# Kernel tuning notes

Hardware: AMD Instinct MI355X
Metric: run time of the kernel (lower is better)

## Reference

```python
import jax, jax.numpy as jnp
import numpy as np

N = 50000      # nodes
E = 1_600_000  # edges
F_IN = 128; HID = 128; LAT = 64; OUT = 128; GEN = 2


def gcn_conv(x, src, dst, norm, W, b, n_nodes):
    """PyG GCNConv with self-loops already appended to (src, dst) and
    symmetric normalization `norm` precomputed per edge."""
    h = x @ W                                    # [N, out]
    msg = h[src] * norm[:, None]                 # [E+N, out] gather + scale
    out = jax.ops.segment_sum(msg, dst, num_segments=n_nodes)
    return out + b


def _self_loop_norm(edge_index, n_nodes):
    loops = jnp.arange(n_nodes, dtype=edge_index.dtype)
    src = jnp.concatenate([edge_index[0], loops])
    dst = jnp.concatenate([edge_index[1], loops])
    deg = jnp.zeros((n_nodes,), jnp.float32).at[dst].add(1.0)
    dinv = jnp.where(deg > 0, deg ** -0.5, 0.0)
    norm = dinv[src] * dinv[dst]
    return src, dst, norm


def setup_inputs() -> dict:
    key = jax.random.key(0)
    ks = jax.random.split(key, 12)
    p = lambda k, s: jax.random.normal(k, s, jnp.float32) * 0.05
    return {
        "x": jax.random.normal(ks[0], (N, F_IN), jnp.float32),
        "edge_index": jax.random.randint(ks[1], (2, E), 0, N, jnp.int32),
        "eps": jax.random.normal(ks[2], (N, LAT), jnp.float32),
        "u": jax.random.uniform(ks[3], (N, GEN), jnp.float32),
        "W1": p(ks[4], (F_IN, HID)), "b1": jnp.zeros((HID,), jnp.float32),
        "W_mu": p(ks[5], (HID, LAT)), "b_mu": jnp.zeros((LAT,), jnp.float32),
        "W_ls": p(ks[6], (HID, LAT)), "b_ls": jnp.zeros((LAT,), jnp.float32),
        "W_dx": p(ks[7], (LAT, OUT)), "b_dx": jnp.zeros((OUT,), jnp.float32),
        "W_g": p(ks[8], (LAT, GEN)), "b_g": jnp.zeros((GEN,), jnp.float32),
        "W_lc": p(ks[9], (LAT, 1)), "b_lc": jnp.zeros((1,), jnp.float32),
    }


def reference(x, edge_index, eps, u, W1, b1, W_mu, b_mu, W_ls, b_ls,
              W_dx, b_dx, W_g, b_g, W_lc, b_lc):
    n = x.shape[0]
    src, dst, norm = _self_loop_norm(edge_index, n)

    # Encoder: GCN -> relu -> (mu, logvar)
    h = jax.nn.relu(gcn_conv(x, src, dst, norm, W1, b1, n))
    mu = gcn_conv(h, src, dst, norm, W_mu, b_mu, n)
    logvar = gcn_conv(h, src, dst, norm, W_ls, b_ls, n)

    # reparameterize: z = eps * exp(0.5*logvar) + mu
    z = eps * jnp.exp(0.5 * logvar) + mu

    # decoders / classifiers
    recon_x = gcn_conv(z, src, dst, norm, W_dx, b_dx, n)
    logits_gender = gcn_conv(z, src, dst, norm, W_g, b_g, n)
    logits_label = z @ W_lc + b_lc

    # Gumbel-softmax (hard, straight-through), temperature=1.0
    g = -jnp.log(-jnp.log(u + 1e-20) + 1e-20)
    y_soft = jax.nn.softmax(logits_gender + g, axis=-1)
    y_hard = jax.nn.one_hot(jnp.argmax(y_soft, axis=-1), GEN, dtype=y_soft.dtype)
    gender = jax.lax.stop_gradient(y_hard - y_soft) + y_soft

    return (recon_x, gender, logits_label, mu, logvar, z)
```

## Files before the change

### kernel.cpp

```cpp
#include <hip/hip_runtime.h>
#include <hip/hip_fp16.h>
#include <cstddef>


constexpr int R = 200;
constexpr int NBUCK = 250;
constexpr int NBLK = 250;
constexpr int SLABCAP = 12288;

__global__ __launch_bounds__(256) void hist_kernel(
    const int* __restrict__ dst, int* __restrict__ gh, int e, int chunk) {
  __shared__ int h[NBUCK];
  for (int t = threadIdx.x; t < NBUCK; t += 256) h[t] = 0;
  __syncthreads();
  int beg = blockIdx.x * chunk;
  int fin = min(e, beg + chunk);
  for (int i = beg + threadIdx.x; i < fin; i += 256)
    atomicAdd(&h[dst[i] / R], 1);
  __syncthreads();
  for (int t = threadIdx.x; t < NBUCK; t += 256)
    gh[t * NBLK + blockIdx.x] = h[t];
}

__global__ void scan_p1(const int* __restrict__ in, int* __restrict__ part, int n) {
  __shared__ int s[256];
  int i = blockIdx.x * 256 + threadIdx.x;
  s[threadIdx.x] = (i < n) ? in[i] : 0;
  __syncthreads();
  for (int off = 128; off > 0; off >>= 1) {
    if (threadIdx.x < off) s[threadIdx.x] += s[threadIdx.x + off];
    __syncthreads();
  }
  if (threadIdx.x == 0) part[blockIdx.x] = s[0];
}

__global__ void scan_p2(int* __restrict__ part, int nb, int* __restrict__ total_out) {
  __shared__ int s[256];
  int v = (threadIdx.x < nb) ? part[threadIdx.x] : 0;
  s[threadIdx.x] = v;
  __syncthreads();
  for (int off = 1; off < 256; off <<= 1) {
    int t = (threadIdx.x >= off) ? s[threadIdx.x - off] : 0;
    __syncthreads();
    s[threadIdx.x] += t;
    __syncthreads();
  }
  if (threadIdx.x < nb) part[threadIdx.x] = s[threadIdx.x] - v;
  if (threadIdx.x == nb - 1) *total_out = s[threadIdx.x];
}

__global__ void scan_p3(int* io, const int* __restrict__ part, int n) {
  __shared__ int s[256];
  int i = blockIdx.x * 256 + threadIdx.x;
  int v = (i < n) ? io[i] : 0;
  s[threadIdx.x] = v;
  __syncthreads();
  for (int off = 1; off < 256; off <<= 1) {
    int t = (threadIdx.x >= off) ? s[threadIdx.x - off] : 0;
    __syncthreads();
    s[threadIdx.x] += t;
    __syncthreads();
  }
  int excl = s[threadIdx.x] - v + part[blockIdx.x];
  if (i < n) io[i] = excl;
}

__global__ __launch_bounds__(256) void scatter_kernel(
    const int* __restrict__ src, const int* __restrict__ dst,
    const int* __restrict__ ghs, int* __restrict__ binned, int e, int chunk) {
  __shared__ int cur[NBUCK];
  for (int t = threadIdx.x; t < NBUCK; t += 256)
    cur[t] = ghs[t * NBLK + blockIdx.x];
  __syncthreads();
  int beg = blockIdx.x * chunk;
  int fin = min(e, beg + chunk);
  for (int i = beg + threadIdx.x; i < fin; i += 256) {
    int d = dst[i];
    int b = d / R;
    int p = atomicAdd(&cur[b], 1);
    binned[p] = ((d - b * R) << 16) | src[i];
  }
}

__global__ __launch_bounds__(256) void final_kernel(
    const int* __restrict__ binned, const int* __restrict__ ghs,
    int* __restrict__ rowptr, int* __restrict__ csr,
    float* __restrict__ dinv, int n, int e) {
  __shared__ int sdeg[R];
  __shared__ int sscan[256];
  __shared__ int scur[R];
  __shared__ int slab[SLABCAP];
  const int b = blockIdx.x;
  const int tid = threadIdx.x;
  const int base = ghs[b * NBLK];
  const int end = (b < NBUCK - 1) ? ghs[(b + 1) * NBLK] : e;
  const int cnt = end - base;

  if (tid < R) sdeg[tid] = 0;
  __syncthreads();
  for (int k = base + tid; k < end; k += 256)
    atomicAdd(&sdeg[binned[k] >> 16], 1);
  __syncthreads();

  int dv = (tid < R) ? sdeg[tid] : 0;
  sscan[tid] = dv;
  __syncthreads();
  for (int off = 1; off < 256; off <<= 1) {
    int t = (tid >= off) ? sscan[tid - off] : 0;
    __syncthreads();
    sscan[tid] += t;
    __syncthreads();
  }
  int excl = sscan[tid] - dv;
  int node = b * R + tid;
  if (tid < R && node < n) {
    rowptr[node] = base + excl;
    dinv[node] = 1.0f / sqrtf((float)dv + 1.0f);
    scur[tid] = excl;
  }
  __syncthreads();

  const bool fits = (cnt <= SLABCAP);
  for (int k = base + tid; k < end; k += 256) {
    int rec = binned[k];
    int p = atomicAdd(&scur[rec >> 16], 1);
    int s = rec & 0xFFFF;
    if (fits) slab[p] = s;
    else csr[base + p] = s;
  }
  __syncthreads();
  if (fits)
    for (int k = tid; k < cnt; k += 256) csr[base + k] = slab[k];
}

template <int K, int M, int KT, int RPT, bool BIAS, bool RELU, bool HALF_OUT>
__global__ __launch_bounds__(256, 4) void gemm_kernel(
    const float* __restrict__ A, const float* __restrict__ W,
    const float* __restrict__ bias, float* __restrict__ C,
    __half* __restrict__ Ch, const float* __restrict__ dinv, int n) {
  constexpr int CG = M / 4;
  constexpr int RS = 256 / CG;
  constexpr int RPB = RS * RPT;
  __shared__ float sW[KT * M];
  const int cg = threadIdx.x % CG;
  const int rs = threadIdx.x / CG;
  const int row0 = blockIdx.x * RPB + rs * RPT;

  const float* Arow[RPT];
#pragma unroll
  for (int rr = 0; rr < RPT; ++rr) {
    int row = row0 + rr;
    if (row > n - 1) row = n - 1;
    Arow[rr] = A + (size_t)row * K;
  }

  float4 acc[RPT];
#pragma unroll
  for (int rr = 0; rr < RPT; ++rr) acc[rr] = float4{0.f, 0.f, 0.f, 0.f};

  for (int kt = 0; kt < K; kt += KT) {
    if (kt) __syncthreads();
    for (int i = threadIdx.x * 4; i < KT * M; i += 1024)
      *reinterpret_cast<float4*>(&sW[i]) =
          *reinterpret_cast<const float4*>(&W[kt * M + i]);
    __syncthreads();
#pragma unroll 4
    for (int k4 = 0; k4 < KT; k4 += 4) {
      float4 a[RPT];
#pragma unroll
      for (int rr = 0; rr < RPT; ++rr)
        a[rr] = *reinterpret_cast<const float4*>(Arow[rr] + kt + k4);
#pragma unroll
      for (int j = 0; j < 4; ++j) {
        float4 w = *reinterpret_cast<const float4*>(&sW[(k4 + j) * M + cg * 4]);
#pragma unroll
        for (int rr = 0; rr < RPT; ++rr) {
          float av = reinterpret_cast<const float*>(&a[rr])[j];
          acc[rr].x += av * w.x;
          acc[rr].y += av * w.y;
          acc[rr].z += av * w.z;
          acc[rr].w += av * w.w;
        }
      }
    }
  }

  float4 bv = float4{0.f, 0.f, 0.f, 0.f};
  if (BIAS) bv = *reinterpret_cast<const float4*>(&bias[cg * 4]);
#pragma unroll
  for (int rr = 0; rr < RPT; ++rr) {
    int row = row0 + rr;
    if (row < n) {
      float4 o = acc[rr];
      if (BIAS) { o.x += bv.x; o.y += bv.y; o.z += bv.z; o.w += bv.w; }
      if (RELU) {
        o.x = fmaxf(o.x, 0.f); o.y = fmaxf(o.y, 0.f);
        o.z = fmaxf(o.z, 0.f); o.w = fmaxf(o.w, 0.f);
      }
      if (HALF_OUT) {
        float di = dinv[row];
        __half2* dst = reinterpret_cast<__half2*>(Ch + (size_t)row * M + cg * 4);
        dst[0] = __floats2half2_rn(di * o.x, di * o.y);
        dst[1] = __floats2half2_rn(di * o.z, di * o.w);
      } else {
        *reinterpret_cast<float4*>(&C[(size_t)row * M + cg * 4]) = o;
      }
    }
  }
}

#if defined(__has_builtin) && __has_builtin(__builtin_amdgcn_fdot2)
typedef _Float16 h2vec __attribute__((ext_vector_type(2)));
__device__ __forceinline__ void dot2acc(__half2 v, float& a0, float& a1) {
  h2vec hv = __builtin_bit_cast(h2vec, v);
  const h2vec e0 = {(_Float16)1.0f, (_Float16)0.0f};
  const h2vec e1 = {(_Float16)0.0f, (_Float16)1.0f};
  a0 = __builtin_amdgcn_fdot2(hv, e0, a0, false);
  a1 = __builtin_amdgcn_fdot2(hv, e1, a1, false);
}
#else
__device__ __forceinline__ void dot2acc(__half2 v, float& a0, float& a1) {
  float2 f = __half22float2(v);
  a0 += f.x;
  a1 += f.y;
}
#endif

template <bool BIAS, bool RELU, bool HALF_OUT>
__global__ __launch_bounds__(256) void spmm128_kernel(
    const __half* __restrict__ Xs, void* __restrict__ Yout,
    const int* __restrict__ rowptr, const int* __restrict__ csr,
    const float* __restrict__ dinv, const float* __restrict__ bias, int n) {
  int wid = (blockIdx.x * blockDim.x + threadIdx.x) >> 6;
  int lane = threadIdx.x & 63;
  if (wid >= n) return;
  int beg = rowptr[wid];
  int end = rowptr[wid + 1];
  constexpr int U = 16;
  constexpr int NA = 8;
  float a0[NA], a1[NA];
#pragma unroll
  for (int uu = 0; uu < NA; ++uu) { a0[uu] = 0.f; a1[uu] = 0.f; }

  for (int base = beg; base < end; base += 64) {
    int m = end - base;
    if (m > 64) m = 64;
    int idx = (lane < m) ? csr[base + lane] : 0;
    int j = 0;
    for (; j + U <= m; j += U) {
      const __half2* rows[U];
#pragma unroll
      for (int uu = 0; uu < U; ++uu) {
        int sidx = __builtin_amdgcn_readlane(idx, j + uu);
        rows[uu] = reinterpret_cast<const __half2*>(Xs + (size_t)sidx * 128);
      }
      __half2 v[U];
#pragma unroll
      for (int uu = 0; uu < U; ++uu) v[uu] = rows[uu][lane];
#pragma unroll
      for (int uu = 0; uu < U; ++uu)
        dot2acc(v[uu], a0[uu & (NA - 1)], a1[uu & (NA - 1)]);
    }
    for (; j < m; ++j) {
      int sidx = __builtin_amdgcn_readlane(idx, j);
      const __half2* row =
          reinterpret_cast<const __half2*>(Xs + (size_t)sidx * 128);
      dot2acc(row[lane], a0[0], a1[0]);
    }
  }

  float t0 = 0.f, t1 = 0.f;
#pragma unroll
  for (int uu = 0; uu < NA; ++uu) { t0 += a0[uu]; t1 += a1[uu]; }

  float2 sf = __half22float2(
      reinterpret_cast<const __half2*>(Xs + (size_t)wid * 128)[lane]);
  t0 += sf.x;
  t1 += sf.y;

  float di = dinv[wid];
  float r0 = di * t0;
  float r1 = di * t1;
  if (BIAS) { r0 += bias[lane * 2]; r1 += bias[lane * 2 + 1]; }
  if (RELU) { r0 = fmaxf(r0, 0.f); r1 = fmaxf(r1, 0.f); }

  if (HALF_OUT) {
    reinterpret_cast<__half2*>((__half*)Yout + (size_t)wid * 128)[lane] =
        __floats2half2_rn(di * r0, di * r1);
  } else {
    float2 o = {r0, r1};
    reinterpret_cast<float2*>((float*)Yout + (size_t)wid * 128)[lane] = o;
  }
}

__global__ __launch_bounds__(256, 4) void mlz_kernel(
    const float* __restrict__ hagg,
    const float* __restrict__ Wmu, const float* __restrict__ bmu,
    const float* __restrict__ Wls, const float* __restrict__ bls,
    const float* __restrict__ eps, const float* __restrict__ dinv,
    const float* __restrict__ Wg, const float* __restrict__ Wlc,
    const float* __restrict__ blc,
    float* __restrict__ out_mu, float* __restrict__ out_lv,
    float* __restrict__ out_z, unsigned int* __restrict__ zh8,
    float2* __restrict__ zgs, float* __restrict__ out_label, int n) {
  constexpr int K = 128, M = 64, KT = 64, RPT = 4;
  constexpr int CG = M / 4;
  constexpr int RS = 256 / CG;
  constexpr int RPB = RS * RPT;
  __shared__ float sWm[KT * M];
  __shared__ float sWl[KT * M];
  const int cg = threadIdx.x % CG;
  const int rs = threadIdx.x / CG;
  const int row0 = blockIdx.x * RPB + rs * RPT;

  const float* Arow[RPT];
#pragma unroll
  for (int rr = 0; rr < RPT; ++rr) {
    int row = row0 + rr;
    if (row > n - 1) row = n - 1;
    Arow[rr] = hagg + (size_t)row * K;
  }

  float4 am[RPT], al[RPT];
#pragma unroll
  for (int rr = 0; rr < RPT; ++rr) {
    am[rr] = float4{0.f, 0.f, 0.f, 0.f};
    al[rr] = float4{0.f, 0.f, 0.f, 0.f};
  }

  for (int kt = 0; kt < K; kt += KT) {
    if (kt) __syncthreads();
    for (int i = threadIdx.x * 4; i < KT * M; i += 1024) {
      *reinterpret_cast<float4*>(&sWm[i]) =
          *reinterpret_cast<const float4*>(&Wmu[kt * M + i]);
      *reinterpret_cast<float4*>(&sWl[i]) =
          *reinterpret_cast<const float4*>(&Wls[kt * M + i]);
    }
    __syncthreads();
#pragma unroll 2
    for (int k4 = 0; k4 < KT; k4 += 4) {
      float4 a[RPT];
#pragma unroll
      for (int rr = 0; rr < RPT; ++rr)
        a[rr] = *reinterpret_cast<const float4*>(Arow[rr] + kt + k4);
#pragma unroll
      for (int j = 0; j < 4; ++j) {
        float4 wm = *reinterpret_cast<const float4*>(&sWm[(k4 + j) * M + cg * 4]);
        float4 wl = *reinterpret_cast<const float4*>(&sWl[(k4 + j) * M + cg * 4]);
#pragma unroll
        for (int rr = 0; rr < RPT; ++rr) {
          float av = reinterpret_cast<const float*>(&a[rr])[j];
          am[rr].x += av * wm.x; am[rr].y += av * wm.y;
          am[rr].z += av * wm.z; am[rr].w += av * wm.w;
          al[rr].x += av * wl.x; al[rr].y += av * wl.y;
          al[rr].z += av * wl.z; al[rr].w += av * wl.w;
        }
      }
    }
  }

  float4 bm = *reinterpret_cast<const float4*>(&bmu[cg * 4]);
  float4 bl = *reinterpret_cast<const float4*>(&bls[cg * 4]);
  float wg0[4], wg1[4], wlcv[4];
#pragma unroll
  for (int cc = 0; cc < 4; ++cc) {
    int c = cg * 4 + cc;
    wg0[cc] = Wg[c * 2 + 0];
    wg1[cc] = Wg[c * 2 + 1];
    wlcv[cc] = Wlc[c];
  }
  float blc0 = blc[0];

#pragma unroll
  for (int rr = 0; rr < RPT; ++rr) {
    int row = row0 + rr;
    if (row < n) {
      float4 mu4 = {am[rr].x + bm.x, am[rr].y + bm.y,
                    am[rr].z + bm.z, am[rr].w + bm.w};
      float4 lv4 = {al[rr].x + bl.x, al[rr].y + bl.y,
                    al[rr].z + bl.z, al[rr].w + bl.w};
      float4 e4 = *reinterpret_cast<const float4*>(&eps[(size_t)row * 64 + cg * 4]);
      float4 z4 = {e4.x * expf(0.5f * lv4.x) + mu4.x,
                   e4.y * expf(0.5f * lv4.y) + mu4.y,
                   e4.z * expf(0.5f * lv4.z) + mu4.z,
                   e4.w * expf(0.5f * lv4.w) + mu4.w};
      *reinterpret_cast<float4*>(&out_mu[(size_t)row * 64 + cg * 4]) = mu4;
      *reinterpret_cast<float4*>(&out_lv[(size_t)row * 64 + cg * 4]) = lv4;
      *reinterpret_cast<float4*>(&out_z[(size_t)row * 64 + cg * 4]) = z4;
      float di = dinv[row];
      int pw = __builtin_amdgcn_cvt_pk_fp8_f32(di * z4.x, di * z4.y, 0, false);
      pw = __builtin_amdgcn_cvt_pk_fp8_f32(di * z4.z, di * z4.w, pw, true);
      zh8[(size_t)row * 16 + cg] = (unsigned int)pw;
      float pg0 = z4.x * wg0[0] + z4.y * wg0[1] + z4.z * wg0[2] + z4.w * wg0[3];
      float pg1 = z4.x * wg1[0] + z4.y * wg1[1] + z4.z * wg1[2] + z4.w * wg1[3];
      float pl  = z4.x * wlcv[0] + z4.y * wlcv[1] + z4.z * wlcv[2] + z4.w * wlcv[3];
#pragma unroll
      for (int off = 1; off < 16; off <<= 1) {
        pg0 += __shfl_xor(pg0, off, 64);
        pg1 += __shfl_xor(pg1, off, 64);
        pl  += __shfl_xor(pl, off, 64);
      }
      if (cg == 0) {
        zgs[row] = float2{di * pg0, di * pg1};
        out_label[row] = pl + blc0;
      }
    }
  }
}

__global__ __launch_bounds__(256) void spmm_zg_kernel(
    const unsigned char* __restrict__ zh8, const float2* __restrict__ zgs,
    float* __restrict__ zagg, const int* __restrict__ rowptr,
    const int* __restrict__ csr, const float* __restrict__ dinv,
    const float* __restrict__ bg, const float* __restrict__ u,
    float* __restrict__ out_gender, int n) {
  int wid = (blockIdx.x * blockDim.x + threadIdx.x) >> 6;
  int lane = threadIdx.x & 63;
  if (wid >= n) return;
  int beg = rowptr[wid];
  int end = rowptr[wid + 1];
  constexpr int U = 16;
  constexpr int NA = 8;
  float acc[NA];
#pragma unroll
  for (int uu = 0; uu < NA; ++uu) acc[uu] = 0.f;
  float ga0 = 0.f, ga1 = 0.f;

  for (int base = beg; base < end; base += 64) {
    int m = end - base;
    if (m > 64) m = 64;
    int idx = 0;
    if (lane < m) {
      idx = csr[base + lane];
      float2 g = zgs[idx];
      ga0 += g.x;
      ga1 += g.y;
    }
    int j = 0;
    for (; j + U <= m; j += U) {
      const unsigned char* rows[U];
#pragma unroll
      for (int uu = 0; uu < U; ++uu)
        rows[uu] =
            zh8 + (size_t)__builtin_amdgcn_readlane(idx, j + uu) * 64;
      int b[U];
#pragma unroll
      for (int uu = 0; uu < U; ++uu) b[uu] = (int)rows[uu][lane];
#pragma unroll
      for (int uu = 0; uu < U; ++uu)
        acc[uu & (NA - 1)] += __builtin_amdgcn_cvt_f32_fp8(b[uu], 0);
    }
    for (; j < m; ++j) {
      const unsigned char* row =
          zh8 + (size_t)__builtin_amdgcn_readlane(idx, j) * 64;
      acc[0] += __builtin_amdgcn_cvt_f32_fp8((int)row[lane], 0);
    }
  }

  float t = 0.f;
#pragma unroll
  for (int uu = 0; uu < NA; ++uu) t += acc[uu];
  t += __builtin_amdgcn_cvt_f32_fp8((int)zh8[(size_t)wid * 64 + lane], 0);

  float di = dinv[wid];
  zagg[(size_t)wid * 64 + lane] = di * t;

  for (int off = 32; off > 0; off >>= 1) {
    ga0 += __shfl_xor(ga0, off, 64);
    ga1 += __shfl_xor(ga1, off, 64);
  }
  if (lane == 0) {
    float2 self = zgs[wid];
    ga0 += self.x;
    ga1 += self.y;
    float lg0 = di * ga0 + bg[0];
    float lg1 = di * ga1 + bg[1];
    float u0 = u[(size_t)wid * 2 + 0];
    float u1 = u[(size_t)wid * 2 + 1];
    float g0 = -logf(-logf(u0 + 1e-20f) + 1e-20f);
    float g1 = -logf(-logf(u1 + 1e-20f) + 1e-20f);
    float a0 = lg0 + g0, a1 = lg1 + g1;
    float mx = fmaxf(a0, a1);
    float e0 = expf(a0 - mx), e1 = expf(a1 - mx);
    float s = e0 + e1;
    float y0 = e0 / s, y1 = e1 / s;
    float h0 = (y1 > y0) ? 0.f : 1.f;
    float h1 = 1.f - h0;
    out_gender[(size_t)wid * 2 + 0] = (h0 - y0) + y0;
    out_gender[(size_t)wid * 2 + 1] = (h1 - y1) + y1;
  }
}

extern "C" void kernel_launch(void* const* d_in, const int* in_sizes, int n_in,
                              void* d_out, int out_size, void* d_ws, size_t ws_size,
                              hipStream_t stream) {
  const float* x   = (const float*)d_in[0];
  const int*   ei  = (const int*)d_in[1];
  const float* eps = (const float*)d_in[2];
  const float* u   = (const float*)d_in[3];
  const float* W1  = (const float*)d_in[4];
  const float* b1  = (const float*)d_in[5];
  const float* Wmu = (const float*)d_in[6];
  const float* bmu = (const float*)d_in[7];
  const float* Wls = (const float*)d_in[8];
  const float* bls = (const float*)d_in[9];
  const float* Wdx = (const float*)d_in[10];
  const float* bdx = (const float*)d_in[11];
  const float* Wg  = (const float*)d_in[12];
  const float* bg  = (const float*)d_in[13];
  const float* Wlc = (const float*)d_in[14];
  const float* blc = (const float*)d_in[15];

  const int n = in_sizes[0] / 128;
  const int e = in_sizes[1] / 2;
  const int* esrc = ei;
  const int* edst = ei + e;

  float* out = (float*)d_out;
  float* out_recon  = out;
  float* out_gender = out + (size_t)n * 128;
  float* out_label  = out_gender + (size_t)n * 2;
  float* out_mu     = out_label + n;
  float* out_lv     = out_mu + (size_t)n * 64;
  float* out_z      = out_lv + (size_t)n * 64;

  char* w = (char*)d_ws;
  size_t off = 0;
  auto alloc = [&](size_t bytes) {
    char* p = w + off;
    off = (off + bytes + 255) & ~(size_t)255;
    return p;
  };
  float* dinv  = (float*)alloc((size_t)n * 4);
  int* rowptr  = (int*)alloc((size_t)(n + 1) * 4);
  int* part    = (int*)alloc(256 * 4);
  int* csr     = (int*)alloc((size_t)e * 4);
  int* gh      = (int*)alloc((size_t)NBUCK * NBLK * 4);
  __half* Xs   = (__half*)alloc((size_t)n * 128 * 2);
  __half* hb   = (__half*)alloc((size_t)n * 128 * 2);
  float2* zgs  = (float2*)alloc((size_t)n * 8);
  unsigned char* zh8 = (unsigned char*)Xs;
  float* zagg  = (float*)hb;
  float* hagg  = out_recon;
  int* binned  = (int*)out_lv;

  const int GH = NBUCK * NBLK;
  const int GHB = (GH + 255) / 256;
  const int chunk = (e + NBLK - 1) / NBLK;

  hist_kernel<<<NBLK, 256, 0, stream>>>(edst, gh, e, chunk);
  scan_p1<<<GHB, 256, 0, stream>>>(gh, part, GH);
  scan_p2<<<1, 256, 0, stream>>>(part, GHB, &rowptr[n]);
  scan_p3<<<GHB, 256, 0, stream>>>(gh, part, GH);
  scatter_kernel<<<NBLK, 256, 0, stream>>>(esrc, edst, gh, binned, e, chunk);
  final_kernel<<<NBUCK, 256, 0, stream>>>(binned, gh, rowptr, csr, dinv, n, e);

  gemm_kernel<128, 128, 64, 4, false, false, true>
      <<<(n + 31) / 32, 256, 0, stream>>>(x, W1, nullptr, nullptr, Xs, dinv, n);
  spmm128_kernel<true, true, true>
      <<<(n + 3) / 4, 256, 0, stream>>>(Xs, hb, rowptr, csr, dinv, b1, n);
  spmm128_kernel<false, false, false>
      <<<(n + 3) / 4, 256, 0, stream>>>(hb, hagg, rowptr, csr, dinv, nullptr, n);
  mlz_kernel<<<(n + 63) / 64, 256, 0, stream>>>(
      hagg, Wmu, bmu, Wls, bls, eps, dinv, Wg, Wlc, blc,
      out_mu, out_lv, out_z, (unsigned int*)zh8, zgs, out_label, n);
  spmm_zg_kernel<<<(n + 3) / 4, 256, 0, stream>>>(
      zh8, (const float2*)zgs, zagg, rowptr, csr, dinv, bg, u, out_gender, n);
  gemm_kernel<64, 128, 64, 4, true, false, false>
      <<<(n + 31) / 32, 256, 0, stream>>>(zagg, Wdx, bdx, out_recon, nullptr, nullptr, n);
}
```

Baseline: 421.6 us.

## Widen per-lane gather loads in SpMM kernels to process multiple neighbor rows per wave

Both SpMM kernels now have each lane load a wider chunk of a neighbor row: 8 bytes of fp16 in the 128-wide kernel and 4 fp8 bytes in the 64-wide kernel. As a result one wave gathers two or four neighbor rows per instruction instead of one. Partial sums from the lane groups are then combined with cross-lane xor shuffles, and the final bias/relu/store runs on a subset of lanes with vector stores. The goal is fewer, wider memory instructions and less per-element conversion overhead in these gather-bound kernels. The cost is extra shuffles, half-idle lanes in the epilogue, and a masked tail path for leftover edges.

Result: no change. 417.0 us (-1.1%).

```diff
diff --git a/kernel.cpp b/kernel.cpp
--- a/kernel.cpp
+++ b/kernel.cpp
@@ -236,60 +236,91 @@
   if (wid >= n) return;
   int beg = rowptr[wid];
   int end = rowptr[wid + 1];
-  constexpr int U = 16;
-  constexpr int NA = 8;
-  float a0[NA], a1[NA];
-#pragma unroll
-  for (int uu = 0; uu < NA; ++uu) { a0[uu] = 0.f; a1[uu] = 0.f; }
+  const int g = lane >> 5;
+  const int c = lane & 31;
+  const int boff = c * 8;
+  const char* __restrict__ Xb = reinterpret_cast<const char*>(Xs);
+
+  float acc[4][4];
+#pragma unroll
+  for (int k = 0; k < 4; ++k)
+#pragma unroll
+    for (int f = 0; f < 4; ++f) acc[k][f] = 0.f;
 
   for (int base = beg; base < end; base += 64) {
     int m = end - base;
     if (m > 64) m = 64;
     int idx = (lane < m) ? csr[base + lane] : 0;
     int j = 0;
-    for (; j + U <= m; j += U) {
-      const __half2* rows[U];
-#pragma unroll
-      for (int uu = 0; uu < U; ++uu) {
-        int sidx = __builtin_amdgcn_readlane(idx, j + uu);
-        rows[uu] = reinterpret_cast<const __half2*>(Xs + (size_t)sidx * 128);
-      }
-      __half2 v[U];
-#pragma unroll
-      for (int uu = 0; uu < U; ++uu) v[uu] = rows[uu][lane];
-#pragma unroll
-      for (int uu = 0; uu < U; ++uu)
-        dot2acc(v[uu], a0[uu & (NA - 1)], a1[uu & (NA - 1)]);
+    for (; j + 16 <= m; j += 16) {
+#pragma unroll
+      for (int s = 0; s < 8; ++s) {
+        int i = __shfl(idx, j + 2 * s + g, 64);
+        uint2 d = *reinterpret_cast<const uint2*>(
+            Xb + ((size_t)(unsigned)i * 256 + boff));
+        __half2 lo = *reinterpret_cast<__half2*>(&d.x);
+        __half2 hi = *reinterpret_cast<__half2*>(&d.y);
+        dot2acc(lo, acc[s & 3][0], acc[s & 3][1]);
+        dot2acc(hi, acc[s & 3][2], acc[s & 3][3]);
+      }
     }
     for (; j < m; ++j) {
-      int sidx = __builtin_amdgcn_readlane(idx, j);
-      const __half2* row =
-          reinterpret_cast<const __half2*>(Xs + (size_t)sidx * 128);
-      dot2acc(row[lane], a0[0], a1[0]);
-    }
-  }
-
-  float t0 = 0.f, t1 = 0.f;
-#pragma unroll
-  for (int uu = 0; uu < NA; ++uu) { t0 += a0[uu]; t1 += a1[uu]; }
-
-  float2 sf = __half22float2(
-      reinterpret_cast<const __half2*>(Xs + (size_t)wid * 128)[lane]);
-  t0 += sf.x;
-  t1 += sf.y;
-
-  float di = dinv[wid];
-  float r0 = di * t0;
-  float r1 = di * t1;
-  if (BIAS) { r0 += bias[lane * 2]; r1 += bias[lane * 2 + 1]; }
-  if (RELU) { r0 = fmaxf(r0, 0.f); r1 = fmaxf(r1, 0.f); }
-
-  if (HALF_OUT) {
-    reinterpret_cast<__half2*>((__half*)Yout + (size_t)wid * 128)[lane] =
-        __floats2half2_rn(di * r0, di * r1);
-  } else {
-    float2 o = {r0, r1};
-    reinterpret_cast<float2*>((float*)Yout + (size_t)wid * 128)[lane] = o;
+      int i = __shfl(idx, j, 64);
+      if (lane < 32) {
+        uint2 d = *reinterpret_cast<const uint2*>(
+            Xb + ((size_t)(unsigned)i * 256 + boff));
+        __half2 lo = *reinterpret_cast<__half2*>(&d.x);
+        __half2 hi = *reinterpret_cast<__half2*>(&d.y);
+        dot2acc(lo, acc[0][0], acc[0][1]);
+        dot2acc(hi, acc[0][2], acc[0][3]);
+      }
+    }
+  }
+
+  float t[4];
+#pragma unroll
+  for (int f = 0; f < 4; ++f) {
+    float p1 = __shfl_xor(acc[0][f], 32, 64);
+    float p3 = __shfl_xor(acc[1][f], 32, 64);
+    float p5 = __shfl_xor(acc[2][f], 32, 64);
+    float p7 = __shfl_xor(acc[3][f], 32, 64);
+    float tt = acc[0][f] + p1;
+    tt += acc[1][f]; tt += p3;
+    tt += acc[2][f]; tt += p5;
+    tt += acc[3][f]; tt += p7;
+    t[f] = tt;
+  }
+
+  if (lane < 32) {
+    uint2 sd = *reinterpret_cast<const uint2*>(
+        Xb + ((size_t)wid * 256 + boff));
+    float2 sl = __half22float2(*reinterpret_cast<__half2*>(&sd.x));
+    float2 sh = __half22float2(*reinterpret_cast<__half2*>(&sd.y));
+    t[0] += sl.x; t[1] += sl.y; t[2] += sh.x; t[3] += sh.y;
+
+    float di = dinv[wid];
+    float r[4];
+#pragma unroll
+    for (int f = 0; f < 4; ++f) r[f] = di * t[f];
+    if (BIAS) {
+      float4 bv = *reinterpret_cast<const float4*>(&bias[4 * c]);
+      r[0] += bv.x; r[1] += bv.y; r[2] += bv.z; r[3] += bv.w;
+    }
+    if (RELU) {
+      r[0] = fmaxf(r[0], 0.f); r[1] = fmaxf(r[1], 0.f);
+      r[2] = fmaxf(r[2], 0.f); r[3] = fmaxf(r[3], 0.f);
+    }
+    if (HALF_OUT) {
+      __half2 h0 = __floats2half2_rn(di * r[0], di * r[1]);
+      __half2 h1 = __floats2half2_rn(di * r[2], di * r[3]);
+      uint2 o;
+      o.x = *reinterpret_cast<unsigned*>(&h0);
+      o.y = *reinterpret_cast<unsigned*>(&h1);
+      *reinterpret_cast<uint2*>((char*)Yout + ((size_t)wid * 256 + boff)) = o;
+    } else {
+      float4 o = {r[0], r[1], r[2], r[3]};
+      *reinterpret_cast<float4*>((float*)Yout + (size_t)wid * 128 + 4 * c) = o;
+    }
   }
 }
 
@@ -408,6 +439,20 @@
   }
 }
 
+__device__ __forceinline__ void fp8x4acc(unsigned d, float* a) {
+#if defined(__has_builtin) && __has_builtin(__builtin_amdgcn_cvt_pk_f32_fp8)
+  typedef float f32x2 __attribute__((ext_vector_type(2)));
+  f32x2 lo = __builtin_amdgcn_cvt_pk_f32_fp8((int)d, false);
+  f32x2 hi = __builtin_amdgcn_cvt_pk_f32_fp8((int)d, true);
+  a[0] += lo.x; a[1] += lo.y; a[2] += hi.x; a[3] += hi.y;
+#else
+  a[0] += __builtin_amdgcn_cvt_f32_fp8((int)d, 0);
+  a[1] += __builtin_amdgcn_cvt_f32_fp8((int)d, 1);
+  a[2] += __builtin_amdgcn_cvt_f32_fp8((int)d, 2);
+  a[3] += __builtin_amdgcn_cvt_f32_fp8((int)d, 3);
+#endif
+}
+
 __global__ __launch_bounds__(256) void spmm_zg_kernel(
     const unsigned char* __restrict__ zh8, const float2* __restrict__ zgs,
     float* __restrict__ zagg, const int* __restrict__ rowptr,
@@ -419,11 +464,13 @@
   if (wid >= n) return;
   int beg = rowptr[wid];
   int end = rowptr[wid + 1];
-  constexpr int U = 16;
-  constexpr int NA = 8;
-  float acc[NA];
-#pragma unroll
-  for (int uu = 0; uu < NA; ++uu) acc[uu] = 0.f;
+  const int g = lane >> 4;
+  const int c = lane & 15;
+  const int coff = c * 4;
+
+  float accA[4], accB[4];
+#pragma unroll
+  for (int f = 0; f < 4; ++f) { accA[f] = 0.f; accB[f] = 0.f; }
   float ga0 = 0.f, ga1 = 0.f;
 
   for (int base = beg; base < end; base += 64) {
@@ -432,38 +479,53 @@
     int idx = 0;
     if (lane < m) {
       idx = csr[base + lane];
-      float2 g = zgs[idx];
-      ga0 += g.x;
-      ga1 += g.y;
+      float2 gz = zgs[idx];
+      ga0 += gz.x;
+      ga1 += gz.y;
     }
     int j = 0;
-    for (; j + U <= m; j += U) {
-      const unsigned char* rows[U];
-#pragma unroll
-      for (int uu = 0; uu < U; ++uu)
-        rows[uu] =
-            zh8 + (size_t)__builtin_amdgcn_readlane(idx, j + uu) * 64;
-      int b[U];
-#pragma unroll
-      for (int uu = 0; uu < U; ++uu) b[uu] = (int)rows[uu][lane];
-#pragma unroll
-      for (int uu = 0; uu < U; ++uu)
-        acc[uu & (NA - 1)] += __builtin_amdgcn_cvt_f32_fp8(b[uu], 0);
-    }
-    for (; j < m; ++j) {
-      const unsigned char* row =
-          zh8 + (size_t)__builtin_amdgcn_readlane(idx, j) * 64;
-      acc[0] += __builtin_amdgcn_cvt_f32_fp8((int)row[lane], 0);
-    }
-  }
-
-  float t = 0.f;
-#pragma unroll
-  for (int uu = 0; uu < NA; ++uu) t += acc[uu];
-  t += __builtin_amdgcn_cvt_f32_fp8((int)zh8[(size_t)wid * 64 + lane], 0);
+    for (; j + 8 <= m; j += 8) {
+      int i0 = __shfl(idx, j + g, 64);
+      int i1 = __shfl(idx, j + 4 + g, 64);
+      unsigned d0 = *reinterpret_cast<const unsigned*>(
+          zh8 + (size_t)(unsigned)i0 * 64 + coff);
+      unsigned d1 = *reinterpret_cast<const unsigned*>(
+          zh8 + (size_t)(unsigned)i1 * 64 + coff);
+      fp8x4acc(d0, accA);
+      fp8x4acc(d1, accB);
+    }
+    if (j < m) {
+      int e0 = j + g;
+      int e1 = j + 4 + g;
+      int i0 = __shfl(idx, min(e0, m - 1), 64);
+      int i1 = __shfl(idx, min(e1, m - 1), 64);
+      unsigned d0 = *reinterpret_cast<const unsigned*>(
+          zh8 + (size_t)(unsigned)i0 * 64 + coff);
+      unsigned d1 = *reinterpret_cast<const unsigned*>(
+          zh8 + (size_t)(unsigned)i1 * 64 + coff);
+      if (e0 >= m) d0 = 0u;
+      if (e1 >= m) d1 = 0u;
+      fp8x4acc(d0, accA);
+      fp8x4acc(d1, accB);
+    }
+  }
+
+  float t[4];
+#pragma unroll
+  for (int f = 0; f < 4; ++f) t[f] = accA[f] + accB[f];
+#pragma unroll
+  for (int f = 0; f < 4; ++f) t[f] += __shfl_xor(t[f], 16, 64);
+#pragma unroll
+  for (int f = 0; f < 4; ++f) t[f] += __shfl_xor(t[f], 32, 64);
 
   float di = dinv[wid];
-  zagg[(size_t)wid * 64 + lane] = di * t;
+  if (lane < 16) {
+    unsigned ds = *reinterpret_cast<const unsigned*>(
+        zh8 + (size_t)wid * 64 + coff);
+    fp8x4acc(ds, t);
+    float4 o = {di * t[0], di * t[1], di * t[2], di * t[3]};
+    *reinterpret_cast<float4*>(&zagg[(size_t)wid * 64 + 4 * c]) = o;
+  }
 
   for (int off = 32; off > 0; off >>= 1) {
     ga0 += __shfl_xor(ga0, off, 64);
```
